# Optimization experiments

Hardware: AMD Instinct MI355X
Metric: run time of the kernel (lower is better)

## Reference

```python
import jax, jax.numpy as jnp
import numpy as np

N, IN_DIM, H1, H2, LIN, MAX_INDEX = 16384, 64, 256, 256, 64, 256


def _init_layer(key, out_dim, in_dim):
    # mimic kaiming_uniform(a=sqrt(5)) + uniform bias bound = 1/sqrt(fan_in)
    kW, kb = jax.random.split(key)
    bound_w = 1.0 / np.sqrt(in_dim)  # gain*sqrt(3/fan_in) with a=sqrt(5) -> 1/sqrt(fan_in)
    W = jax.random.uniform(kW, (MAX_INDEX, out_dim, in_dim), jnp.float32, -bound_w, bound_w)
    b = jax.random.uniform(kb, (MAX_INDEX, out_dim), jnp.float32, -bound_w, bound_w)
    return W, b


def setup_inputs() -> dict:
    key = jax.random.key(0)
    kx, ki, k1, k2, k3 = jax.random.split(key, 5)
    x = jax.random.normal(kx, (N, IN_DIM), jnp.float32)
    ind = jax.random.randint(ki, (N,), 0, MAX_INDEX, jnp.int64 if jax.config.jax_enable_x64 else jnp.int32)
    W1, b1 = _init_layer(k1, H1, IN_DIM)
    W2, b2 = _init_layer(k2, H2, H1)
    Wl, bl = _init_layer(k3, LIN, H2)
    return {"x": x, "ind": ind, "W1": W1, "b1": b1, "W2": W2, "b2": b2, "Wl": Wl, "bl": bl}


def _index_linear(x, ind, W, b):
    # per-row expert weight gather then row-wise matvec: out[n] = W[ind[n]] @ x[n] + b[ind[n]]
    return jnp.einsum('noi,ni->no', W[ind], x) + b[ind]


def reference(x, ind, W1, b1, W2, b2, Wl, bl):
    h = jnp.tanh(_index_linear(x, ind, W1, b1))
    h = jnp.tanh(_index_linear(h, ind, W2, b2))
    return _index_linear(h, ind, Wl, bl)
```

## Files before the change

### kernel.cpp

```cpp
#include <hip/hip_runtime.h>
#include <hip/hip_bf16.h>
#include <math.h>

#define NROWS   16384
#define IN_DIM  64
#define HID     256
#define OUT_DIM 64
#define NEXP    256
#define MT      112
#define HP      264

typedef __attribute__((ext_vector_type(8))) short short8;
typedef __attribute__((ext_vector_type(4))) float f32x4;
typedef __attribute__((ext_vector_type(4))) unsigned uint4v;
typedef __attribute__((ext_vector_type(2))) unsigned uint2v;


__global__ __launch_bounds__(1024) void prep_k(const int* __restrict__ ind,
                                               int* __restrict__ rows,
                                               int* __restrict__ offsets) {
  __shared__ int hist[NEXP];
  __shared__ int scan[NEXP];
  __shared__ int cur[NEXP];
  int t = threadIdx.x;
  if (t < NEXP) hist[t] = 0;
  __syncthreads();
  for (int n = t; n < NROWS; n += 1024) atomicAdd(&hist[ind[n]], 1);
  __syncthreads();
  if (t < NEXP) scan[t] = hist[t];
  __syncthreads();
  for (int d = 1; d < NEXP; d <<= 1) {
    int v = (t < NEXP && t >= d) ? scan[t - d] : 0;
    __syncthreads();
    if (t < NEXP) scan[t] += v;
    __syncthreads();
  }
  if (t < NEXP) {
    int exc = scan[t] - hist[t];
    offsets[t] = exc;
    cur[t] = exc;
    if (t == NEXP - 1) offsets[NEXP] = scan[t];
  }
  __syncthreads();
  for (int n = t; n < NROWS; n += 1024) {
    int p = atomicAdd(&cur[ind[n]], 1);
    rows[p] = n;
  }
}


__device__ __forceinline__ unsigned pk2_trunc(float a, float b) {
  unsigned ua = __builtin_bit_cast(unsigned, a);
  unsigned ub = __builtin_bit_cast(unsigned, b);
  return (ub & 0xffff0000u) | (ua >> 16);
}

__device__ __forceinline__ unsigned pk2_rn(float a, float b) {
  __hip_bfloat162 h = __float22bfloat162_rn(float2{a, b});
  unsigned r;
  __builtin_memcpy(&r, &h, 4);
  return r;
}

__device__ __forceinline__ short8 cvt8w(f32x4 w0, f32x4 w1) {
  uint4v u;
  u.x = pk2_trunc(w0.x, w0.y);
  u.y = pk2_trunc(w0.z, w0.w);
  u.z = pk2_trunc(w1.x, w1.y);
  u.w = pk2_trunc(w1.z, w1.w);
  return __builtin_bit_cast(short8, u);
}

__device__ __forceinline__ float fast_tanh(float v) {
  float e = __expf(2.f * v);
  return 1.f - 2.f * __builtin_amdgcn_rcpf(e + 1.f);
}

template <int K, int NNT>
__device__ __forceinline__ void layer_mm1(const float* __restrict__ wr,
                                          f32x4 bv,
                                          const unsigned short* __restrict__ Hin,
                                          int l15, int q, f32x4 (&acc)[NNT]) {
  constexpr int KS = K / 32;
#pragma unroll
  for (int nt = 0; nt < NNT; nt++) acc[nt] = bv;
  f32x4 wbuf[3][2];
  wbuf[0][0] = *(const f32x4*)(wr);
  wbuf[0][1] = *(const f32x4*)(wr + 4);
  if (KS > 1) {
    wbuf[1][0] = *(const f32x4*)(wr + 32);
    wbuf[1][1] = *(const f32x4*)(wr + 36);
  }
#pragma unroll
  for (int ks = 0; ks < KS; ks++) {
    if (ks + 2 < KS) {
      wbuf[(ks + 2) % 3][0] = *(const f32x4*)(wr + (ks + 2) * 32);
      wbuf[(ks + 2) % 3][1] = *(const f32x4*)(wr + (ks + 2) * 32 + 4);
    }
    short8 a = cvt8w(wbuf[ks % 3][0], wbuf[ks % 3][1]);
#pragma unroll
    for (int nt = 0; nt < NNT; nt++) {
      short8 b = *(const short8*)&Hin[(nt * 16 + l15) * HP + ks * 32 + q * 8];
      acc[nt] = __builtin_amdgcn_mfma_f32_16x16x32_bf16(a, b, acc[nt], 0, 0, 0);
    }
  }
}

template <int NNT>
__device__ __forceinline__ void write_h1(f32x4 (&acc)[NNT], unsigned short* H,
                                         int col, int l15) {
#pragma unroll
  for (int nt = 0; nt < NNT; nt++) {
    uint2v v;
    v.x = pk2_rn(fast_tanh(acc[nt].x), fast_tanh(acc[nt].y));
    v.y = pk2_rn(fast_tanh(acc[nt].z), fast_tanh(acc[nt].w));
    *(uint2v*)&H[(nt * 16 + l15) * HP + col] = v;
  }
}


__global__ __launch_bounds__(1024, 4) void mlp_k(
    const float* __restrict__ x,
    const float* __restrict__ W1, const float* __restrict__ b1,
    const float* __restrict__ W2, const float* __restrict__ b2,
    const float* __restrict__ Wl, const float* __restrict__ bl,
    const int* __restrict__ rows, const int* __restrict__ offsets,
    float* __restrict__ out) {
  __shared__ __align__(16) unsigned short H[MT * HP];

  const int t = threadIdx.x;
  const int w = t >> 6;
  const int l15 = t & 15;
  const int q = (t >> 4) & 3;
  const int e = blockIdx.x;
  const int beg = offsets[e];
  const int cnt = offsets[e + 1] - beg;

  const float* W1e = W1 + (size_t)e * HID * IN_DIM + (size_t)(w * 16 + l15) * IN_DIM + q * 8;
  const float* W2e = W2 + (size_t)e * HID * HID + (size_t)(w * 16 + l15) * HID + q * 8;
  const int m3 = w & 3;
  const int ntA = w >> 2;
  const int nt1 = (ntA + 4 < 7) ? ntA + 4 : 6;
  const float* Wle = Wl + (size_t)e * OUT_DIM * HID + (size_t)(m3 * 16 + l15) * HID + q * 8;
  const f32x4 b1v = *(const f32x4*)(b1 + e * HID + w * 16 + q * 4);
  const f32x4 b2v = *(const f32x4*)(b2 + e * HID + w * 16 + q * 4);
  const f32x4 blv = *(const f32x4*)(bl + e * OUT_DIM + m3 * 16 + q * 4);

  const int sm = t >> 3;
  const int sc = (t & 7) * 8;

  for (int mt0 = 0; mt0 < cnt; mt0 += MT) {
    if (mt0) __syncthreads();
    if (sm < MT) {
      int gm = mt0 + sm;
      bool val = gm < cnt;
      int r = val ? rows[beg + gm] : 0;
      const float* xr = x + (size_t)r * IN_DIM + sc;
      uint4v u;
      if (val) {
        f32x4 a0 = *(const f32x4*)(xr);
        f32x4 a1 = *(const f32x4*)(xr + 4);
        u.x = pk2_rn(a0.x, a0.y); u.y = pk2_rn(a0.z, a0.w);
        u.z = pk2_rn(a1.x, a1.y); u.w = pk2_rn(a1.z, a1.w);
      } else {
        u = (uint4v){0, 0, 0, 0};
      }
      *(uint4v*)&H[sm * HP + sc] = u;
    }
    __syncthreads();

    {
      f32x4 acc[7];
      layer_mm1<IN_DIM, 7>(W1e, b1v, H, l15, q, acc);
      __syncthreads();
      write_h1<7>(acc, H, w * 16 + q * 4, l15);
    }
    __syncthreads();

    {
      f32x4 acc[7];
      layer_mm1<HID, 7>(W2e, b2v, H, l15, q, acc);
      __syncthreads();
      write_h1<7>(acc, H, w * 16 + q * 4, l15);
    }
    __syncthreads();

    {
      f32x4 acc[2];
      acc[0] = blv; acc[1] = blv;
      f32x4 wbuf[3][2];
      wbuf[0][0] = *(const f32x4*)(Wle);
      wbuf[0][1] = *(const f32x4*)(Wle + 4);
      wbuf[1][0] = *(const f32x4*)(Wle + 32);
      wbuf[1][1] = *(const f32x4*)(Wle + 36);
#pragma unroll
      for (int ks = 0; ks < 8; ks++) {
        if (ks + 2 < 8) {
          wbuf[(ks + 2) % 3][0] = *(const f32x4*)(Wle + (ks + 2) * 32);
          wbuf[(ks + 2) % 3][1] = *(const f32x4*)(Wle + (ks + 2) * 32 + 4);
        }
        short8 a = cvt8w(wbuf[ks % 3][0], wbuf[ks % 3][1]);
        short8 bA = *(const short8*)&H[(ntA * 16 + l15) * HP + ks * 32 + q * 8];
        short8 bB = *(const short8*)&H[(nt1 * 16 + l15) * HP + ks * 32 + q * 8];
        acc[0] = __builtin_amdgcn_mfma_f32_16x16x32_bf16(a, bA, acc[0], 0, 0, 0);
        acc[1] = __builtin_amdgcn_mfma_f32_16x16x32_bf16(a, bB, acc[1], 0, 0, 0);
      }
      {
        int gm = mt0 + ntA * 16 + l15;
        if (gm < cnt) {
          int r = rows[beg + gm];
          *(f32x4*)(out + (size_t)r * OUT_DIM + m3 * 16 + q * 4) = acc[0];
        }
      }
      if (ntA + 4 < 7) {
        int gm = mt0 + nt1 * 16 + l15;
        if (gm < cnt) {
          int r = rows[beg + gm];
          *(f32x4*)(out + (size_t)r * OUT_DIM + m3 * 16 + q * 4) = acc[1];
        }
      }
    }
  }
}


extern "C" void kernel_launch(void* const* d_in, const int* in_sizes, int n_in,
                              void* d_out, int out_size, void* d_ws, size_t ws_size,
                              hipStream_t stream) {
  const float* x   = (const float*)d_in[0];
  const int*   ind = (const int*)d_in[1];
  const float* W1  = (const float*)d_in[2];
  const float* b1  = (const float*)d_in[3];
  const float* W2  = (const float*)d_in[4];
  const float* b2  = (const float*)d_in[5];
  const float* Wl  = (const float*)d_in[6];
  const float* bl  = (const float*)d_in[7];
  float* out = (float*)d_out;

  int* offsets = (int*)d_ws;
  int* rows    = (int*)d_ws + 260;

  prep_k<<<1, 1024, 0, stream>>>(ind, rows, offsets);
  mlp_k<<<NEXP, 1024, 0, stream>>>(x, W1, b1, W2, b2, Wl, bl, rows, offsets, out);
}
```

Baseline: 171.1 us.

## Preload full expert weights before barriers and specialize tile count per expert

All W1 and W2 weight fragments are loaded into registers before the x staging and barriers, and Wl is loaded during layer 2, replacing the three-deep rolling prefetch. The aim is to hide global weight latency behind the x gather and the layer-1 work. The tile body is templated on the number of 16-row tiles actually present (4 to 7), so experts with fewer rows skip MFMAs and LDS reads on empty tiles. Weight truncation now uses a single byte-permute instruction. The larger register footprint for the preloaded weights risks spilling or reduced occupancy under the 1024-thread launch bound, and the four instantiations increase code size.

```diff
diff --git a/kernel.cpp b/kernel.cpp
--- a/kernel.cpp
+++ b/kernel.cpp
@@ -50,9 +50,8 @@
 
 
 __device__ __forceinline__ unsigned pk2_trunc(float a, float b) {
-  unsigned ua = __builtin_bit_cast(unsigned, a);
-  unsigned ub = __builtin_bit_cast(unsigned, b);
-  return (ub & 0xffff0000u) | (ua >> 16);
+  return __builtin_amdgcn_perm(__builtin_bit_cast(unsigned, b),
+                               __builtin_bit_cast(unsigned, a), 0x07060302u);
 }
 
 __device__ __forceinline__ unsigned pk2_rn(float a, float b) {
@@ -76,28 +75,25 @@
   return 1.f - 2.f * __builtin_amdgcn_rcpf(e + 1.f);
 }
 
+template <int KS>
+__device__ __forceinline__ void wload(f32x4 (&wb)[KS][2], const float* __restrict__ wr) {
+#pragma unroll
+  for (int ks = 0; ks < KS; ks++) {
+    wb[ks][0] = *(const f32x4*)(wr + ks * 32);
+    wb[ks][1] = *(const f32x4*)(wr + ks * 32 + 4);
+  }
+}
+
 template <int K, int NNT>
-__device__ __forceinline__ void layer_mm1(const float* __restrict__ wr,
-                                          f32x4 bv,
-                                          const unsigned short* __restrict__ Hin,
-                                          int l15, int q, f32x4 (&acc)[NNT]) {
+__device__ __forceinline__ void layer_mfma(const f32x4 (&wb)[K / 32][2], f32x4 bv,
+                                           const unsigned short* __restrict__ Hin,
+                                           int l15, int q, f32x4 (&acc)[NNT]) {
   constexpr int KS = K / 32;
 #pragma unroll
   for (int nt = 0; nt < NNT; nt++) acc[nt] = bv;
-  f32x4 wbuf[3][2];
-  wbuf[0][0] = *(const f32x4*)(wr);
-  wbuf[0][1] = *(const f32x4*)(wr + 4);
-  if (KS > 1) {
-    wbuf[1][0] = *(const f32x4*)(wr + 32);
-    wbuf[1][1] = *(const f32x4*)(wr + 36);
-  }
 #pragma unroll
   for (int ks = 0; ks < KS; ks++) {
-    if (ks + 2 < KS) {
-      wbuf[(ks + 2) % 3][0] = *(const f32x4*)(wr + (ks + 2) * 32);
-      wbuf[(ks + 2) % 3][1] = *(const f32x4*)(wr + (ks + 2) * 32 + 4);
-    }
-    short8 a = cvt8w(wbuf[ks % 3][0], wbuf[ks % 3][1]);
+    short8 a = cvt8w(wb[ks][0], wb[ks][1]);
 #pragma unroll
     for (int nt = 0; nt < NNT; nt++) {
       short8 b = *(const short8*)&Hin[(nt * 16 + l15) * HP + ks * 32 + q * 8];
@@ -115,6 +111,80 @@
     v.x = pk2_rn(fast_tanh(acc[nt].x), fast_tanh(acc[nt].y));
     v.y = pk2_rn(fast_tanh(acc[nt].z), fast_tanh(acc[nt].w));
     *(uint2v*)&H[(nt * 16 + l15) * HP + col] = v;
+  }
+}
+
+
+template <int NNT>
+__device__ __forceinline__ void tile_body(
+    const float* __restrict__ W1e, const float* __restrict__ W2e,
+    const float* __restrict__ Wle,
+    f32x4 b1v, f32x4 b2v, f32x4 blv,
+    unsigned short* __restrict__ H, int l15, int q, int w,
+    int m3, int ntA,
+    const int* __restrict__ rows, int beg, int cnt, int mt0,
+    const float* __restrict__ x, float* __restrict__ out, int sm, int sc) {
+  f32x4 w1b[2][2], w2b[8][2];
+  wload<2>(w1b, W1e);
+  wload<8>(w2b, W2e);
+
+  if (sm < MT) {
+    int gm = mt0 + sm;
+    bool val = gm < cnt;
+    int r = val ? rows[beg + gm] : 0;
+    const float* xr = x + (size_t)r * IN_DIM + sc;
+    uint4v u;
+    if (val) {
+      f32x4 a0 = *(const f32x4*)(xr);
+      f32x4 a1 = *(const f32x4*)(xr + 4);
+      u.x = pk2_rn(a0.x, a0.y); u.y = pk2_rn(a0.z, a0.w);
+      u.z = pk2_rn(a1.x, a1.y); u.w = pk2_rn(a1.z, a1.w);
+    } else {
+      u = (uint4v){0, 0, 0, 0};
+    }
+    *(uint4v*)&H[sm * HP + sc] = u;
+  }
+  __syncthreads();
+
+  f32x4 acc[NNT];
+  layer_mfma<IN_DIM, NNT>(w1b, b1v, H, l15, q, acc);
+  __syncthreads();
+  write_h1<NNT>(acc, H, w * 16 + q * 4, l15);
+  __syncthreads();
+
+  layer_mfma<HID, NNT>(w2b, b2v, H, l15, q, acc);
+  f32x4 wlb[8][2];
+  wload<8>(wlb, Wle);
+  __syncthreads();
+  write_h1<NNT>(acc, H, w * 16 + q * 4, l15);
+  __syncthreads();
+
+  {
+    const int ntB = (ntA + 4 < NNT) ? ntA + 4 : 0;
+    f32x4 a3[2];
+    a3[0] = blv; a3[1] = blv;
+#pragma unroll
+    for (int ks = 0; ks < 8; ks++) {
+      short8 a = cvt8w(wlb[ks][0], wlb[ks][1]);
+      short8 bA = *(const short8*)&H[(ntA * 16 + l15) * HP + ks * 32 + q * 8];
+      short8 bB = *(const short8*)&H[(ntB * 16 + l15) * HP + ks * 32 + q * 8];
+      a3[0] = __builtin_amdgcn_mfma_f32_16x16x32_bf16(a, bA, a3[0], 0, 0, 0);
+      a3[1] = __builtin_amdgcn_mfma_f32_16x16x32_bf16(a, bB, a3[1], 0, 0, 0);
+    }
+    {
+      int gm = mt0 + ntA * 16 + l15;
+      if (gm < cnt) {
+        int r = rows[beg + gm];
+        *(f32x4*)(out + (size_t)r * OUT_DIM + m3 * 16 + q * 4) = a3[0];
+      }
+    }
+    if (ntA + 4 < NNT) {
+      int gm = mt0 + (ntA + 4) * 16 + l15;
+      if (gm < cnt) {
+        int r = rows[beg + gm];
+        *(f32x4*)(out + (size_t)r * OUT_DIM + m3 * 16 + q * 4) = a3[1];
+      }
+    }
   }
 }
 
@@ -140,7 +210,6 @@
   const float* W2e = W2 + (size_t)e * HID * HID + (size_t)(w * 16 + l15) * HID + q * 8;
   const int m3 = w & 3;
   const int ntA = w >> 2;
-  const int nt1 = (ntA + 4 < 7) ? ntA + 4 : 6;
   const float* Wle = Wl + (size_t)e * OUT_DIM * HID + (size_t)(m3 * 16 + l15) * HID + q * 8;
   const f32x4 b1v = *(const f32x4*)(b1 + e * HID + w * 16 + q * 4);
   const f32x4 b2v = *(const f32x4*)(b2 + e * HID + w * 16 + q * 4);
@@ -151,75 +220,21 @@
 
   for (int mt0 = 0; mt0 < cnt; mt0 += MT) {
     if (mt0) __syncthreads();
-    if (sm < MT) {
-      int gm = mt0 + sm;
-      bool val = gm < cnt;
-      int r = val ? rows[beg + gm] : 0;
-      const float* xr = x + (size_t)r * IN_DIM + sc;
-      uint4v u;
-      if (val) {
-        f32x4 a0 = *(const f32x4*)(xr);
-        f32x4 a1 = *(const f32x4*)(xr + 4);
-        u.x = pk2_rn(a0.x, a0.y); u.y = pk2_rn(a0.z, a0.w);
-        u.z = pk2_rn(a1.x, a1.y); u.w = pk2_rn(a1.z, a1.w);
-      } else {
-        u = (uint4v){0, 0, 0, 0};
-      }
-      *(uint4v*)&H[sm * HP + sc] = u;
-    }
-    __syncthreads();
-
-    {
-      f32x4 acc[7];
-      layer_mm1<IN_DIM, 7>(W1e, b1v, H, l15, q, acc);
-      __syncthreads();
-      write_h1<7>(acc, H, w * 16 + q * 4, l15);
-    }
-    __syncthreads();
-
-    {
-      f32x4 acc[7];
-      layer_mm1<HID, 7>(W2e, b2v, H, l15, q, acc);
-      __syncthreads();
-      write_h1<7>(acc, H, w * 16 + q * 4, l15);
-    }
-    __syncthreads();
-
-    {
-      f32x4 acc[2];
-      acc[0] = blv; acc[1] = blv;
-      f32x4 wbuf[3][2];
-      wbuf[0][0] = *(const f32x4*)(Wle);
-      wbuf[0][1] = *(const f32x4*)(Wle + 4);
-      wbuf[1][0] = *(const f32x4*)(Wle + 32);
-      wbuf[1][1] = *(const f32x4*)(Wle + 36);
-#pragma unroll
-      for (int ks = 0; ks < 8; ks++) {
-        if (ks + 2 < 8) {
-          wbuf[(ks + 2) % 3][0] = *(const f32x4*)(Wle + (ks + 2) * 32);
-          wbuf[(ks + 2) % 3][1] = *(const f32x4*)(Wle + (ks + 2) * 32 + 4);
-        }
-        short8 a = cvt8w(wbuf[ks % 3][0], wbuf[ks % 3][1]);
-        short8 bA = *(const short8*)&H[(ntA * 16 + l15) * HP + ks * 32 + q * 8];
-        short8 bB = *(const short8*)&H[(nt1 * 16 + l15) * HP + ks * 32 + q * 8];
-        acc[0] = __builtin_amdgcn_mfma_f32_16x16x32_bf16(a, bA, acc[0], 0, 0, 0);
-        acc[1] = __builtin_amdgcn_mfma_f32_16x16x32_bf16(a, bB, acc[1], 0, 0, 0);
-      }
-      {
-        int gm = mt0 + ntA * 16 + l15;
-        if (gm < cnt) {
-          int r = rows[beg + gm];
-          *(f32x4*)(out + (size_t)r * OUT_DIM + m3 * 16 + q * 4) = acc[0];
-        }
-      }
-      if (ntA + 4 < 7) {
-        int gm = mt0 + nt1 * 16 + l15;
-        if (gm < cnt) {
-          int r = rows[beg + gm];
-          *(f32x4*)(out + (size_t)r * OUT_DIM + m3 * 16 + q * 4) = acc[1];
-        }
-      }
-    }
+    int rem = cnt - mt0;
+    if (rem > MT) rem = MT;
+    int ntiles = (rem + 15) >> 4;
+    if (ntiles <= 4)
+      tile_body<4>(W1e, W2e, Wle, b1v, b2v, blv, H, l15, q, w, m3, ntA,
+                   rows, beg, cnt, mt0, x, out, sm, sc);
+    else if (ntiles == 5)
+      tile_body<5>(W1e, W2e, Wle, b1v, b2v, blv, H, l15, q, w, m3, ntA,
+                   rows, beg, cnt, mt0, x, out, sm, sc);
+    else if (ntiles == 6)
+      tile_body<6>(W1e, W2e, Wle, b1v, b2v, blv, H, l15, q, w, m3, ntA,
+                   rows, beg, cnt, mt0, x, out, sm, sc);
+    else
+      tile_body<7>(W1e, W2e, Wle, b1v, b2v, blv, H, l15, q, w, m3, ntA,
+                   rows, beg, cnt, mt0, x, out, sm, sc);
   }
 }
 
```

Measured after the change: 171.1 us. Within noise of the previous version (+0.0%).
